# Kernel optimization log

Hardware: AMD Instinct MI355X
Metric: run time of the kernel (lower is better)

Reference implementation:

```python
import jax, jax.numpy as jnp
import numpy as np

HID = 64  # self.hidden_num

def setup_inputs() -> dict:
    key = jax.random.key(0)
    ks = jax.random.split(key, 6)
    B, C_IN, N, T, C_OUT = 2, 64, 128, 24, 64
    x = jax.random.normal(ks[0], (B, C_IN, N, T), dtype=jnp.float32)
    attention = jax.random.uniform(ks[1], (B, 1, N, N, T), dtype=jnp.float32)
    # agg_fc1: Linear(c_in, 64); agg_fc2: Linear(128, c_out). Store weights as [in, out].
    s1 = 1.0 / np.sqrt(C_IN)
    s2 = 1.0 / np.sqrt(2 * HID)
    W1 = jax.random.uniform(ks[2], (C_IN, HID), jnp.float32, -s1, s1)
    b1 = jax.random.uniform(ks[3], (HID,), jnp.float32, -s1, s1)
    W2 = jax.random.uniform(ks[4], (2 * HID, C_OUT), jnp.float32, -s2, s2)
    b2 = jax.random.uniform(ks[5], (C_OUT,), jnp.float32, -s2, s2)
    return {"x": x, "attention": attention, "W1": W1, "b1": b1, "W2": W2, "b2": b2}

def reference(x, attention, W1, b1, W2, b2):
    # x: [B, H, N, T] -> [B, N, T, H]
    xp = jnp.transpose(x, (0, 2, 3, 1))
    h = xp @ W1 + b1  # [B, N, T, HID]
    # Original: concat(v_feature, h_feature) @ W2 where v=h_i (dim 1=dest i), h=h_j (dim 2=src j).
    # Exact decomposition: message[b,i,j,t] = h[b,i,t]@W2v + h[b,j,t]@W2h + b2,
    # avoiding the O(N^2) concat tensor.
    mv = h @ W2[:HID]   # [B, N, T, C_OUT] (dest part)
    mh = h @ W2[HID:]   # [B, N, T, C_OUT] (src part)
    a = attention[:, 0]  # [B, N(i), N(j), T]
    asum = jnp.sum(a, axis=2)  # [B, N, T]
    upd = asum[..., None] * (mv + b2) + jnp.einsum('bijt,bjtc->bitc', a, mh)
    return jnp.transpose(upd, (0, 3, 1, 2))  # [B, C_OUT, N, T]
```

## Files before the change

### kernel.cpp

```cpp
#include <hip/hip_runtime.h>

constexpr int B_   = 2;
constexpr int CIN  = 64;
constexpr int N    = 128;
constexpr int T    = 24;
constexpr int HID  = 64;
constexpr int COUT = 64;
constexpr int NT   = N * T;
constexpr int BT   = B_ * T;
constexpr int ATT_BLOCKS = B_ * N;
constexpr int XT_BLOCKS  = 32;
constexpr int WF_BLOCKS  = 16;
constexpr int PREP_BLOCKS = ATT_BLOCKS + XT_BLOCKS + WF_BLOCKS;

typedef __attribute__((ext_vector_type(8))) short short8;
typedef __attribute__((ext_vector_type(4))) float f32x4;

__device__ inline unsigned short f2bf(float f) {
    unsigned u = __float_as_uint(f);
    return (unsigned short)((u + 0x7FFFu + ((u >> 16) & 1u)) >> 16);
}

__global__ __launch_bounds__(256) void k_prep(
    const float* __restrict__ x,
    const float* __restrict__ att,
    const float* __restrict__ W1,
    const float* __restrict__ b1,
    const float* __restrict__ W2,
    const float* __restrict__ b2,
    unsigned* __restrict__ xT32,
    unsigned* __restrict__ attT32,
    float* __restrict__ asum_g,
    unsigned short* __restrict__ WfvT,
    unsigned short* __restrict__ WfhT,
    float* __restrict__ bvb2,
    float* __restrict__ bh)
{
    __shared__ __align__(16) unsigned smem_u32[8320];
    const int tid = threadIdx.x;
    const int blk = blockIdx.x;

    if (blk < ATT_BLOCKS) {
        float* ts   = (float*)smem_u32;
        float* psum = ts + 3200;
        const int b = blk >> 7;
        const int i = blk & 127;

        const float* ab = att + ((size_t)b * N + i) * NT;
#pragma unroll
        for (int u = 0; u < 12; ++u) {
            const int idx = tid + 256 * u;
            const int j = idx / T, t = idx - j * T;
            ts[j * 25 + t] = ab[idx];
        }
        __syncthreads();
#pragma unroll
        for (int u = 0; u < 6; ++u) {
            const int e2 = tid + 256 * u;
            const int t = e2 >> 6, jp = e2 & 63, j = jp * 2;
            const unsigned pk = (unsigned)f2bf(ts[j * 25 + t])
                              | ((unsigned)f2bf(ts[(j + 1) * 25 + t]) << 16);
            attT32[((size_t)(b * T + t) * N + i) * 64 + jp] = pk;
        }
        if (tid < 192) {
            const int t = tid >> 3, p = tid & 7;
            float s = 0.f;
#pragma unroll
            for (int q = 0; q < 16; ++q) s += ts[(p * 16 + q) * 25 + t];
            psum[t * 8 + p] = s;
        }
        __syncthreads();
        if (tid < T) {
            float s = 0.f;
#pragma unroll
            for (int p = 0; p < 8; ++p) s += psum[tid * 8 + p];
            asum_g[(size_t)(b * T + tid) * N + i] = s;
        }
    } else if (blk < ATT_BLOCKS + XT_BLOCKS) {
        const int tb = blk - ATT_BLOCKS;
        const int b  = tb >> 4;
        const int n0 = (tb & 15) * 8;
#pragma unroll
        for (int u = 0; u < 12; ++u) {
            const int vidx = tid + 256 * u;
            const int cp = vidx / 48, w48 = vidx - cp * 48;
            const float4 v = *(const float4*)(x + (size_t)(b * CIN + cp) * NT
                                              + n0 * T + w48 * 4);
            smem_u32[cp * 97 + w48 * 2]     = (unsigned)f2bf(v.x) | ((unsigned)f2bf(v.y) << 16);
            smem_u32[cp * 97 + w48 * 2 + 1] = (unsigned)f2bf(v.z) | ((unsigned)f2bf(v.w) << 16);
        }
        __syncthreads();
#pragma unroll
        for (int v = 0; v < 24; ++v) {
            const int oidx = tid + 256 * v;
            const int t = oidx >> 8, rem = oidx & 255;
            const int n = rem >> 5, cp = rem & 31;
            const int r = n * T + t;
            const unsigned w0 = smem_u32[(2 * cp) * 97 + (r >> 1)];
            const unsigned w1 = smem_u32[(2 * cp + 1) * 97 + (r >> 1)];
            const unsigned v0 = (r & 1) ? (w0 >> 16) : (w0 & 0xFFFFu);
            const unsigned v1 = (r & 1) ? (w1 >> 16) : (w1 & 0xFFFFu);
            xT32[((size_t)(b * T + t) * N + n0 + n) * 32 + cp] = v0 | (v1 << 16);
        }
    } else {
        const int wf   = blk - (ATT_BLOCKS + XT_BLOCKS);
        const int half = wf >> 3;
        const int c0   = (wf & 7) * 8;
        float* sW1 = (float*)smem_u32;
        float* sW2 = sW1 + 64 * 65;
#pragma unroll
        for (int u = 0; u < 16; ++u) {
            const int i = tid + 256 * u;
            const int r = i >> 6, q = i & 63;
            sW1[r * 65 + q] = W1[i];
            sW2[r * 65 + q] = W2[half * 4096 + i];
        }
        __syncthreads();

        const int c = c0 + (tid & 7);
        const int r = tid >> 3;
        float a0 = 0.f, a1 = 0.f;
#pragma unroll
        for (int q = 0; q < 64; ++q) {
            const float w2 = sW2[q * 65 + c];
            a0 += sW1[r * 65 + q] * w2;
            a1 += sW1[(r + 32) * 65 + q] * w2;
        }
        unsigned short* dst = half ? WfhT : WfvT;
        dst[c * 64 + r]      = f2bf(a0);
        dst[c * 64 + r + 32] = f2bf(a1);

        if (tid < 8) {
            const int cb = c0 + tid;
            float s = 0.f;
#pragma unroll
            for (int q = 0; q < 64; ++q) s += b1[q] * sW2[q * 65 + cb];
            if (half) bh[cb] = s;
            else      bvb2[cb] = s + b2[cb];
        }
    }
}

__global__ __launch_bounds__(256) void k_all(
    const unsigned short* __restrict__ xTb,
    const unsigned short* __restrict__ attTb,
    const unsigned short* __restrict__ WfvT,
    const unsigned short* __restrict__ WfhT,
    const float* __restrict__ bvb2,
    const float* __restrict__ bh,
    const float* __restrict__ asum_g,
    float* __restrict__ out)
{
    __shared__ __align__(8) unsigned short mhT[64][140];

    const int blk   = blockIdx.x;
    const int itile = blk & 7;
    const int bt    = blk >> 3;
    const int b     = bt / T;
    const int t     = bt - b * T;

    const int tid  = threadIdx.x;
    const int w    = tid >> 6;
    const int lane = tid & 63;
    const int c16  = lane & 15;
    const int q4   = lane >> 4;
    const int cc   = w * 16 + c16;

    const unsigned short* whr = WfhT + cc * 64;
    const short8 wh0 = *(const short8*)(whr + q4 * 8);
    const short8 wh1 = *(const short8*)(whr + 32 + q4 * 8);
    const unsigned short* wvr = WfvT + cc * 64;
    const short8 wv0 = *(const short8*)(wvr + q4 * 8);
    const short8 wv1 = *(const short8*)(wvr + 32 + q4 * 8);
    const float bhc = bh[cc];
    const float bvc = bvb2[cc];

    const unsigned short* xpanel = xTb + (size_t)bt * N * CIN;

    f32x4 accv = {0.f, 0.f, 0.f, 0.f};
#pragma unroll
    for (int nt8 = 0; nt8 < 8; ++nt8) {
        const unsigned short* xr = xpanel + (nt8 * 16 + c16) * CIN;
        const short8 a0 = *(const short8*)(xr + q4 * 8);
        const short8 a1 = *(const short8*)(xr + 32 + q4 * 8);
        f32x4 d = {0.f, 0.f, 0.f, 0.f};
        d = __builtin_amdgcn_mfma_f32_16x16x32_bf16(a0, wh0, d, 0, 0, 0);
        d = __builtin_amdgcn_mfma_f32_16x16x32_bf16(a1, wh1, d, 0, 0, 0);
        uint2 pk;
        pk.x = (unsigned)f2bf(d[0] + bhc) | ((unsigned)f2bf(d[1] + bhc) << 16);
        pk.y = (unsigned)f2bf(d[2] + bhc) | ((unsigned)f2bf(d[3] + bhc) << 16);
        *(uint2*)&mhT[cc][nt8 * 16 + q4 * 4] = pk;
        if (nt8 == itile) {
            accv = __builtin_amdgcn_mfma_f32_16x16x32_bf16(a0, wv0, accv, 0, 0, 0);
            accv = __builtin_amdgcn_mfma_f32_16x16x32_bf16(a1, wv1, accv, 0, 0, 0);
        }
    }
    __syncthreads();

    f32x4 acc = {0.f, 0.f, 0.f, 0.f};
    const unsigned short* arow = attTb + ((size_t)bt * N + itile * 16 + c16) * N;
#pragma unroll
    for (int ks = 0; ks < 4; ++ks) {
        const short8 a  = *(const short8*)(arow + ks * 32 + q4 * 8);
        const short8 bb = *(const short8*)(&mhT[cc][ks * 32 + q4 * 8]);
        acc = __builtin_amdgcn_mfma_f32_16x16x32_bf16(a, bb, acc, 0, 0, 0);
    }

    const int il0 = itile * 16 + q4 * 4;
    const f32x4 as4 = *(const f32x4*)(asum_g + (size_t)bt * N + il0);
    float* ob = out + (((size_t)b * COUT + cc) * N + il0) * T + t;
#pragma unroll
    for (int e = 0; e < 4; ++e) {
        ob[e * T] = acc[e] + as4[e] * (accv[e] + bvc);
    }
}

extern "C" void kernel_launch(void* const* d_in, const int* in_sizes, int n_in,
                              void* d_out, int out_size, void* d_ws, size_t ws_size,
                              hipStream_t stream)
{
    const float* x   = (const float*)d_in[0];
    const float* att = (const float*)d_in[1];
    const float* W1  = (const float*)d_in[2];
    const float* b1  = (const float*)d_in[3];
    const float* W2  = (const float*)d_in[4];
    const float* b2  = (const float*)d_in[5];
    float* out = (float*)d_out;

    char* ws = (char*)d_ws;
    unsigned*       xT32   = (unsigned*)ws;
    unsigned*       attT32 = (unsigned*)(ws + 786432);
    float*          asum_g = (float*)(ws + 2359296);
    unsigned short* WfvT   = (unsigned short*)(ws + 2383872);
    unsigned short* WfhT   = (unsigned short*)(ws + 2392064);
    float*          bvb2   = (float*)(ws + 2400256);
    float*          bh     = (float*)(ws + 2400512);

    k_prep<<<PREP_BLOCKS, 256, 0, stream>>>(x, att, W1, b1, W2, b2,
                                            xT32, attT32, asum_g,
                                            WfvT, WfhT, bvb2, bh);
    k_all<<<BT * 8, 256, 0, stream>>>((const unsigned short*)xT32,
                                      (const unsigned short*)attT32,
                                      WfvT, WfhT, bvb2, bh, asum_g, out);
}
```

Before: 18.69 us.

## Split mh projection across waves and stage x/attention tiles in LDS

The main kernel now launches 96 blocks of 512 threads, one per (b,t) and half of the destination rows, instead of 384 blocks of 256 threads. Each wave computes a distinct 16-row slice of the mh projection, where before every block recomputed all eight slices redundantly. The x panel and attention half-tile are staged into LDS with coalesced 16-byte loads, and each wave then produces two output channel tiles. This cuts duplicated MFMA work and global reads, but leaves fewer, larger blocks with more LDS each, which may reduce occupancy and latency hiding.

```diff
diff --git a/kernel.cpp b/kernel.cpp
--- a/kernel.cpp
+++ b/kernel.cpp
@@ -12,6 +12,7 @@
 constexpr int XT_BLOCKS  = 32;
 constexpr int WF_BLOCKS  = 16;
 constexpr int PREP_BLOCKS = ATT_BLOCKS + XT_BLOCKS + WF_BLOCKS;
+constexpr int MAIN_BLOCKS = BT * 2;
 
 typedef __attribute__((ext_vector_type(8))) short short8;
 typedef __attribute__((ext_vector_type(4))) float f32x4;
@@ -141,9 +142,9 @@
     }
 }
 
-__global__ __launch_bounds__(256) void k_all(
-    const unsigned short* __restrict__ xTb,
-    const unsigned short* __restrict__ attTb,
+__global__ __launch_bounds__(512) void k_main(
+    const unsigned* __restrict__ xT32,
+    const unsigned* __restrict__ attT32,
     const unsigned short* __restrict__ WfvT,
     const unsigned short* __restrict__ WfhT,
     const float* __restrict__ bvb2,
@@ -151,11 +152,13 @@
     const float* __restrict__ asum_g,
     float* __restrict__ out)
 {
-    __shared__ __align__(8) unsigned short mhT[64][140];
+    __shared__ __align__(16) unsigned x_lds[128][36];
+    __shared__ __align__(16) unsigned att_lds[64][68];
+    __shared__ __align__(16) unsigned short mh_lds[64][136];
 
     const int blk   = blockIdx.x;
-    const int itile = blk & 7;
-    const int bt    = blk >> 3;
+    const int ihalf = blk & 1;
+    const int bt    = blk >> 1;
     const int b     = bt / T;
     const int t     = bt - b * T;
 
@@ -164,54 +167,96 @@
     const int lane = tid & 63;
     const int c16  = lane & 15;
     const int q4   = lane >> 4;
-    const int cc   = w * 16 + c16;
-
-    const unsigned short* whr = WfhT + cc * 64;
-    const short8 wh0 = *(const short8*)(whr + q4 * 8);
-    const short8 wh1 = *(const short8*)(whr + 32 + q4 * 8);
-    const unsigned short* wvr = WfvT + cc * 64;
-    const short8 wv0 = *(const short8*)(wvr + q4 * 8);
-    const short8 wv1 = *(const short8*)(wvr + 32 + q4 * 8);
-    const float bhc = bh[cc];
-    const float bvc = bvb2[cc];
-
-    const unsigned short* xpanel = xTb + (size_t)bt * N * CIN;
-
-    f32x4 accv = {0.f, 0.f, 0.f, 0.f};
-#pragma unroll
-    for (int nt8 = 0; nt8 < 8; ++nt8) {
-        const unsigned short* xr = xpanel + (nt8 * 16 + c16) * CIN;
-        const short8 a0 = *(const short8*)(xr + q4 * 8);
-        const short8 a1 = *(const short8*)(xr + 32 + q4 * 8);
+
+    {
+        const uint4* src = (const uint4*)(xT32 + (size_t)bt * 4096);
+#pragma unroll
+        for (int u = 0; u < 2; ++u) {
+            const int vi = tid + 512 * u;
+            const uint4 v = src[vi];
+            *(uint4*)&x_lds[vi >> 3][(vi & 7) * 4] = v;
+        }
+    }
+    {
+        const uint4* src = (const uint4*)(attT32 + ((size_t)bt * 128 + ihalf * 64) * 64);
+#pragma unroll
+        for (int u = 0; u < 2; ++u) {
+            const int vi = tid + 512 * u;
+            const uint4 v = src[vi];
+            *(uint4*)&att_lds[vi >> 4][(vi & 15) * 4] = v;
+        }
+    }
+
+    const int ct0 = (w >> 2) * 2;
+    short8 wh0[4], wh1[4];
+#pragma unroll
+    for (int ct = 0; ct < 4; ++ct) {
+        wh0[ct] = *(const short8*)(WfhT + (ct * 16 + c16) * 64 + q4 * 8);
+        wh1[ct] = *(const short8*)(WfhT + (ct * 16 + c16) * 64 + 32 + q4 * 8);
+    }
+    short8 wv0[2], wv1[2];
+#pragma unroll
+    for (int p = 0; p < 2; ++p) {
+        wv0[p] = *(const short8*)(WfvT + ((ct0 + p) * 16 + c16) * 64 + q4 * 8);
+        wv1[p] = *(const short8*)(WfvT + ((ct0 + p) * 16 + c16) * 64 + 32 + q4 * 8);
+    }
+    float bhc[4];
+#pragma unroll
+    for (int ct = 0; ct < 4; ++ct) bhc[ct] = bh[ct * 16 + c16];
+    float bvc[2];
+#pragma unroll
+    for (int p = 0; p < 2; ++p) bvc[p] = bvb2[(ct0 + p) * 16 + c16];
+
+    const int il_base = ihalf * 64 + (w & 3) * 16;
+    const f32x4 as4 = *(const f32x4*)(asum_g + (size_t)bt * N + il_base + q4 * 4);
+
+    __syncthreads();
+
+    const short8 a0 = *(const short8*)&x_lds[w * 16 + c16][q4 * 4];
+    const short8 a1 = *(const short8*)&x_lds[w * 16 + c16][16 + q4 * 4];
+    const int nt_mv = ihalf * 4 + (w & 3);
+    const short8 m0 = *(const short8*)&x_lds[nt_mv * 16 + c16][q4 * 4];
+    const short8 m1 = *(const short8*)&x_lds[nt_mv * 16 + c16][16 + q4 * 4];
+
+#pragma unroll
+    for (int ct = 0; ct < 4; ++ct) {
         f32x4 d = {0.f, 0.f, 0.f, 0.f};
-        d = __builtin_amdgcn_mfma_f32_16x16x32_bf16(a0, wh0, d, 0, 0, 0);
-        d = __builtin_amdgcn_mfma_f32_16x16x32_bf16(a1, wh1, d, 0, 0, 0);
+        d = __builtin_amdgcn_mfma_f32_16x16x32_bf16(a0, wh0[ct], d, 0, 0, 0);
+        d = __builtin_amdgcn_mfma_f32_16x16x32_bf16(a1, wh1[ct], d, 0, 0, 0);
         uint2 pk;
-        pk.x = (unsigned)f2bf(d[0] + bhc) | ((unsigned)f2bf(d[1] + bhc) << 16);
-        pk.y = (unsigned)f2bf(d[2] + bhc) | ((unsigned)f2bf(d[3] + bhc) << 16);
-        *(uint2*)&mhT[cc][nt8 * 16 + q4 * 4] = pk;
-        if (nt8 == itile) {
-            accv = __builtin_amdgcn_mfma_f32_16x16x32_bf16(a0, wv0, accv, 0, 0, 0);
-            accv = __builtin_amdgcn_mfma_f32_16x16x32_bf16(a1, wv1, accv, 0, 0, 0);
-        }
-    }
+        pk.x = (unsigned)f2bf(d[0] + bhc[ct]) | ((unsigned)f2bf(d[1] + bhc[ct]) << 16);
+        pk.y = (unsigned)f2bf(d[2] + bhc[ct]) | ((unsigned)f2bf(d[3] + bhc[ct]) << 16);
+        *(uint2*)&mh_lds[ct * 16 + c16][w * 16 + q4 * 4] = pk;
+    }
+    f32x4 dv0 = {0.f, 0.f, 0.f, 0.f}, dv1 = {0.f, 0.f, 0.f, 0.f};
+    dv0 = __builtin_amdgcn_mfma_f32_16x16x32_bf16(m0, wv0[0], dv0, 0, 0, 0);
+    dv0 = __builtin_amdgcn_mfma_f32_16x16x32_bf16(m1, wv1[0], dv0, 0, 0, 0);
+    dv1 = __builtin_amdgcn_mfma_f32_16x16x32_bf16(m0, wv0[1], dv1, 0, 0, 0);
+    dv1 = __builtin_amdgcn_mfma_f32_16x16x32_bf16(m1, wv1[1], dv1, 0, 0, 0);
+
     __syncthreads();
 
-    f32x4 acc = {0.f, 0.f, 0.f, 0.f};
-    const unsigned short* arow = attTb + ((size_t)bt * N + itile * 16 + c16) * N;
+    f32x4 acc0 = {0.f, 0.f, 0.f, 0.f}, acc1 = {0.f, 0.f, 0.f, 0.f};
+    const int ir = (w & 3) * 16 + c16;
 #pragma unroll
     for (int ks = 0; ks < 4; ++ks) {
-        const short8 a  = *(const short8*)(arow + ks * 32 + q4 * 8);
-        const short8 bb = *(const short8*)(&mhT[cc][ks * 32 + q4 * 8]);
-        acc = __builtin_amdgcn_mfma_f32_16x16x32_bf16(a, bb, acc, 0, 0, 0);
-    }
-
-    const int il0 = itile * 16 + q4 * 4;
-    const f32x4 as4 = *(const f32x4*)(asum_g + (size_t)bt * N + il0);
-    float* ob = out + (((size_t)b * COUT + cc) * N + il0) * T + t;
-#pragma unroll
-    for (int e = 0; e < 4; ++e) {
-        ob[e * T] = acc[e] + as4[e] * (accv[e] + bvc);
+        const short8 a  = *(const short8*)&att_lds[ir][ks * 16 + q4 * 4];
+        const short8 b0 = *(const short8*)&mh_lds[ct0 * 16 + c16][ks * 32 + q4 * 8];
+        const short8 b1 = *(const short8*)&mh_lds[(ct0 + 1) * 16 + c16][ks * 32 + q4 * 8];
+        acc0 = __builtin_amdgcn_mfma_f32_16x16x32_bf16(a, b0, acc0, 0, 0, 0);
+        acc1 = __builtin_amdgcn_mfma_f32_16x16x32_bf16(a, b1, acc1, 0, 0, 0);
+    }
+
+    {
+        const int cc0 = ct0 * 16 + c16;
+        const int cc1 = (ct0 + 1) * 16 + c16;
+        float* ob0 = out + (((size_t)b * COUT + cc0) * N + il_base + q4 * 4) * T + t;
+        float* ob1 = out + (((size_t)b * COUT + cc1) * N + il_base + q4 * 4) * T + t;
+#pragma unroll
+        for (int e = 0; e < 4; ++e) {
+            ob0[e * T] = acc0[e] + as4[e] * (dv0[e] + bvc[0]);
+            ob1[e * T] = acc1[e] + as4[e] * (dv1[e] + bvc[1]);
+        }
     }
 }
 
@@ -239,7 +284,6 @@
     k_prep<<<PREP_BLOCKS, 256, 0, stream>>>(x, att, W1, b1, W2, b2,
                                             xT32, attT32, asum_g,
                                             WfvT, WfhT, bvb2, bh);
-    k_all<<<BT * 8, 256, 0, stream>>>((const unsigned short*)xT32,
-                                      (const unsigned short*)attT32,
-                                      WfvT, WfhT, bvb2, bh, asum_g, out);
-}
+    k_main<<<MAIN_BLOCKS, 512, 0, stream>>>(xT32, attT32,
+                                            WfvT, WfhT, bvb2, bh, asum_g, out);
+}
```

Result: no change. 18.55 us (median of 2 runs) (-0.7%).
